# Performance work log

Hardware: AMD Instinct MI355X
Metric: run time of the kernel (lower is better)

## Reference

```python
import jax, jax.numpy as jnp
import numpy as np

SPARSITY = 0.01  # sparsity_threshold (softshrink lambda)


def _cas(n):
    # Hartley cas kernel: cos + sin
    t = jnp.arange(n, dtype=jnp.float32)
    a = 2.0 * jnp.pi * jnp.outer(t, t) / n
    return jnp.cos(a) + jnp.sin(a)


def _dht2d(x):
    # Faithful to source 4-D branch: transforms the LAST TWO axes (W and C)
    B, H, W, C = x.shape
    y = jnp.einsum('bhwc,cd->bhwd', x, _cas(C))          # contract channel axis
    return jnp.einsum('vw,bhwd->bhvd', _cas(W), y)       # contract width axis


def setup_inputs() -> dict:
    key = jax.random.key(0)
    k0, k1, k2, k3, k4 = jax.random.split(key, 5)
    B, H, W, C = 1, 180, 360, 512
    nb, bs, f = 8, 64, 1  # num_blocks, block_size, hidden_size_factor
    scale = 0.02
    x = jax.random.normal(k0, (B, H, W, C), jnp.float32)
    w1 = scale * jax.random.normal(k1, (2, nb, bs, bs * f), jnp.float32)
    b1 = scale * jax.random.normal(k2, (2, nb, bs * f), jnp.float32)
    w2 = scale * jax.random.normal(k3, (2, nb, bs * f, bs), jnp.float32)
    b2 = scale * jax.random.normal(k4, (2, nb, bs), jnp.float32)
    return {"x": x, "w1": w1, "b1": b1, "w2": w2, "b2": b2}


def reference(x, w1, b1, w2, b2):
    bias = x
    B, H, W, C = x.shape
    nb, bs = w1.shape[1], w1.shape[2]

    xh = _dht2d(x).reshape(B, H, W, nb, bs)                       # X_H_k
    xn = jnp.roll(jnp.flip(xh, axis=(1, 2)), shift=(1, 1), axis=(1, 2))  # X_H_{-k}

    # layer 1: 0.5*(Xk(w0+w1) + Xn(w0-w1)) + b  (algebraic regroup of the 4 einsums)
    w1a, w1b = w1[0] + w1[1], w1[0] - w1[1]
    o1k = jax.nn.relu(0.5 * (jnp.einsum('bhwki,kio->bhwko', xh, w1a)
                             + jnp.einsum('bhwki,kio->bhwko', xn, w1b)) + b1[0])
    o1n = jax.nn.relu(0.5 * (jnp.einsum('bhwki,kio->bhwko', xn, w1a)
                             + jnp.einsum('bhwki,kio->bhwko', xh, w1b)) + b1[1])

    # layer 2 (faithfully reproduces source bug: o2n consumes o2k, bias included)
    w2a, w2b = w2[0] + w2[1], w2[0] - w2[1]
    o2k = 0.5 * (jnp.einsum('bhwki,kio->bhwko', o1k, w2a)
                 + jnp.einsum('bhwki,kio->bhwko', o1n, w2b)) + b2[0]
    o2n = 0.5 * (jnp.einsum('bhwki,kio->bhwko', o1n, w2a)
                 + jnp.einsum('bhwki,kio->bhwko', o2k, w2b)) + b2[1]

    y = (o2k + o2n).reshape(B, H, W, C)
    y = jnp.sign(y) * jax.nn.relu(jnp.abs(y) - SPARSITY)          # softshrink
    y = _dht2d(y) / (W * C)                                       # idht2d normalization
    return y + bias
```

## Files before the change

### kernel.cpp

```cpp
#include <hip/hip_runtime.h>
#include <math.h>

#define HH 180
#define WDIM 360
#define CDIM 512
#define NP 64800
#define PL 184320

typedef unsigned short u16;
typedef __attribute__((ext_vector_type(8))) short short8;
typedef __attribute__((ext_vector_type(4))) float f4;

__device__ __forceinline__ u16 f2bf(float f){
    unsigned u = __float_as_uint(f);
    return (u16)((u + 0x7fffu + ((u >> 16) & 1u)) >> 16);
}
__device__ __forceinline__ void gl_lds16(const void* g, void* l){
    __builtin_amdgcn_global_load_lds((const __attribute__((address_space(1))) void*)g,
                                     (__attribute__((address_space(3))) void*)l, 16, 0, 0);
}

__global__ void prep(const float* __restrict__ w1, const float* __restrict__ w2,
                     u16* __restrict__ casC, u16* __restrict__ casW, u16* __restrict__ wts)
{
    int idx = blockIdx.x * 256 + threadIdx.x;
    if (idx < 512*512){
        int i = idx >> 9, j = idx & 511;
        int m = (i * j) & 511;
        float a = (float)m * (6.283185307179586f / 512.0f);
        float s, c; __sincosf(a, &s, &c);
        casC[idx] = f2bf(c + s);
    }
    if (idx < 360*384){
        int i = idx / 384, j = idx - (idx / 384) * 384;
        u16 v = 0;
        if (j < 360){
            int m = (i * j) % 360;
            float a = (float)m * (6.283185307179586f / 360.0f);
            float s, c; __sincosf(a, &s, &c);
            v = f2bf(c + s);
        }
        casW[idx] = v;
    }
    if (idx < 131072){
        int s = idx >> 15, r = idx & 32767;
        int kb = r >> 12, o = (r >> 6) & 63, ii = r & 63;
        const float* w = (s < 2) ? w1 : w2;
        float v0 = w[kb*4096 + ii*64 + o];
        float v1 = w[32768 + kb*4096 + ii*64 + o];
        float v = 0.5f * ((s & 1) ? (v0 - v1) : (v0 + v1));
        wts[idx] = f2bf(v);
    }
}

template<int ASTAGE, int STORE, int SWAP>
__global__ __launch_bounds__(256)
void gemm_k(const void* __restrict__ A, int ldA, long long sA, int clampA,
            const u16* __restrict__ B, int ldB, long long sB,
            void* __restrict__ C, long long sC, int Mreal,
            const float* __restrict__ X, float scale, int nK)
{
    __shared__ u16 As[4096];
    __shared__ u16 Bs[4096];

    const int tid = threadIdx.x, wv = tid >> 6, l = tid & 63;
    const int l16 = l & 15, quad = l >> 4;
    const int z = blockIdx.z;
    const int bx = SWAP ? blockIdx.y : blockIdx.x;
    const int by = SWAP ? blockIdx.x : blockIdx.y;
    const int row0 = bx * 128, col0 = by * 128;

    const int rh = wv & 1, c0 = wv >> 1;

    const u16* gB = B + sB * z + (long long)(col0 + rh*64 + l) * ldB;
    u16* lB0 = Bs + c0*1024 + rh*512;
    u16* lB1 = lB0 + 2048;

    const u16* gA = nullptr; u16* lA0 = nullptr; u16* lA1 = nullptr;
    const float* gAf = nullptr; int arow = 0;
    if constexpr (ASTAGE == 0){
        int r = row0 + rh*64 + l; r = r <= clampA ? r : clampA;
        gA  = (const u16*)A + sA * z + (long long)r * ldA;
        lA0 = As + c0*1024 + rh*512;
        lA1 = lA0 + 2048;
    } else {
        int r = row0 + (tid >> 1); r = r <= clampA ? r : clampA;
        gAf  = (const float*)A + (long long)r * ldA + (tid & 1) * 16;
        arow = tid >> 1;
    }

    f4 acc[4][4];
    #pragma unroll
    for (int mt = 0; mt < 4; ++mt)
        #pragma unroll
        for (int nt = 0; nt < 4; ++nt)
            acc[mt][nt] = (f4)0.0f;

    const int mrow = (wv >> 1) * 64, ncol = (wv & 1) * 64;

    for (int kt = 0; kt < nK; ++kt){
        const int k0 = kt * 32;
        gl_lds16(gB + k0 + c0*8,     lB0);
        gl_lds16(gB + k0 + (c0+2)*8, lB1);
        if constexpr (ASTAGE == 0){
            gl_lds16(gA + k0 + c0*8,     lA0);
            gl_lds16(gA + k0 + (c0+2)*8, lA1);
        } else {
            const float* p = gAf + k0;
            float4 f0 = *(const float4*)(p);
            float4 f1 = *(const float4*)(p + 4);
            float4 f2 = *(const float4*)(p + 8);
            float4 f3 = *(const float4*)(p + 12);
            uint4 w0, w1;
            w0.x = (unsigned)f2bf(f0.x) | ((unsigned)f2bf(f0.y) << 16);
            w0.y = (unsigned)f2bf(f0.z) | ((unsigned)f2bf(f0.w) << 16);
            w0.z = (unsigned)f2bf(f1.x) | ((unsigned)f2bf(f1.y) << 16);
            w0.w = (unsigned)f2bf(f1.z) | ((unsigned)f2bf(f1.w) << 16);
            w1.x = (unsigned)f2bf(f2.x) | ((unsigned)f2bf(f2.y) << 16);
            w1.y = (unsigned)f2bf(f2.z) | ((unsigned)f2bf(f2.w) << 16);
            w1.z = (unsigned)f2bf(f3.x) | ((unsigned)f2bf(f3.y) << 16);
            w1.w = (unsigned)f2bf(f3.z) | ((unsigned)f2bf(f3.w) << 16);
            const int cb = (tid & 1) * 2;
            *(uint4*)&As[cb*1024       + arow*8] = w0;
            *(uint4*)&As[(cb+1)*1024   + arow*8] = w1;
        }
        __syncthreads();
        short8 af[4];
        #pragma unroll
        for (int mt = 0; mt < 4; ++mt)
            af[mt] = *(const short8*)&As[quad*1024 + (mrow + mt*16 + l16)*8];
        #pragma unroll
        for (int nt = 0; nt < 4; ++nt){
            short8 bfv = *(const short8*)&Bs[quad*1024 + (ncol + nt*16 + l16)*8];
            #pragma unroll
            for (int mt = 0; mt < 4; ++mt)
                acc[mt][nt] = __builtin_amdgcn_mfma_f32_16x16x32_bf16(af[mt], bfv, acc[mt][nt], 0, 0, 0);
        }
        __syncthreads();
    }

    #pragma unroll
    for (int mt = 0; mt < 4; ++mt){
        #pragma unroll
        for (int i = 0; i < 4; ++i){
            int gr = row0 + mrow + mt*16 + quad*4 + i;
            if (gr >= Mreal) continue;
            int th = 0, tw = 0;
            if constexpr (STORE == 1){ th = gr / 360; tw = gr - th * 360; }
            #pragma unroll
            for (int nt = 0; nt < 4; ++nt){
                int gc = col0 + ncol + nt*16 + l16;
                if constexpr (STORE == 0){
                    ((u16*)C)[sC*z + (long long)gr*512 + gc] = f2bf(acc[mt][nt][i]);
                } else if constexpr (STORE == 1){
                    ((u16*)C)[((long long)th*512 + gc)*360 + tw] = f2bf(acc[mt][nt][i]);
                } else {
                    long long off = sC*z + (long long)gr*512 + gc;
                    ((float*)C)[off] = fmaf(acc[mt][nt][i], scale, X[off]);
                }
            }
        }
    }
}

__global__ __launch_bounds__(256)
void mlp_k(const u16* __restrict__ xh, const u16* __restrict__ wts,
           const float* __restrict__ b1, const float* __restrict__ b2,
           u16* __restrict__ yout)
{
    __shared__ u16 sW0[64*72], sW1[64*72];
    __shared__ u16 sXh[64*72], sXn[64*72], s1k[64*72], s1n[64*72];
    __shared__ float sb[256];

    const int tid = threadIdx.x;
    const int wv = tid >> 6, l = tid & 63, lane16 = l & 15, quad = l >> 4;
    const int kb = blockIdx.y;
    const int p0 = blockIdx.x * 64;
    const int w16 = wv * 16;

    if (tid < 64){
        sb[tid]       = b1[kb*64 + tid];
        sb[64 + tid]  = b1[512 + kb*64 + tid];
        sb[128 + tid] = b2[kb*64 + tid];
        sb[192 + tid] = b2[512 + kb*64 + tid];
    }
    {
        const int r = tid >> 2, sg = (tid & 3) * 16;
        const u16* s0 = wts + kb*4096 + r*64 + sg;
        const u16* s1 = wts + 32768 + kb*4096 + r*64 + sg;
        *(uint4*)&sW0[r*72 + sg]     = *(const uint4*)s0;
        *(uint4*)&sW0[r*72 + sg + 8] = *(const uint4*)(s0 + 8);
        *(uint4*)&sW1[r*72 + sg]     = *(const uint4*)s1;
        *(uint4*)&sW1[r*72 + sg + 8] = *(const uint4*)(s1 + 8);

        int p = p0 + r; int pc = p <= 64799 ? p : 64799;
        int h = pc / 360; int v = pc - h * 360;
        int hn = (h == 0) ? 0 : (180 - h);
        int vn = (v == 0) ? 0 : (360 - v);
        long long bh = (long long)pc * 512 + kb*64 + sg;
        long long bn = (long long)(hn*360 + vn) * 512 + kb*64 + sg;
        *(uint4*)&sXh[r*72 + sg]     = *(const uint4*)&xh[bh];
        *(uint4*)&sXh[r*72 + sg + 8] = *(const uint4*)&xh[bh + 8];
        *(uint4*)&sXn[r*72 + sg]     = *(const uint4*)&xh[bn];
        *(uint4*)&sXn[r*72 + sg + 8] = *(const uint4*)&xh[bn + 8];
    }
    __syncthreads();

    f4 aK[4], aN[4];
    #pragma unroll
    for (int nt = 0; nt < 4; ++nt){ aK[nt] = (f4)0.0f; aN[nt] = (f4)0.0f; }
    #pragma unroll
    for (int kq = 0; kq < 2; ++kq){
        short8 fxh = *(const short8*)&sXh[(w16 + lane16)*72 + kq*32 + quad*8];
        short8 fxn = *(const short8*)&sXn[(w16 + lane16)*72 + kq*32 + quad*8];
        #pragma unroll
        for (int nt = 0; nt < 4; ++nt){
            short8 wa = *(const short8*)&sW0[(nt*16 + lane16)*72 + kq*32 + quad*8];
            short8 wb = *(const short8*)&sW1[(nt*16 + lane16)*72 + kq*32 + quad*8];
            aK[nt] = __builtin_amdgcn_mfma_f32_16x16x32_bf16(fxh, wa, aK[nt], 0,0,0);
            aK[nt] = __builtin_amdgcn_mfma_f32_16x16x32_bf16(fxn, wb, aK[nt], 0,0,0);
            aN[nt] = __builtin_amdgcn_mfma_f32_16x16x32_bf16(fxn, wa, aN[nt], 0,0,0);
            aN[nt] = __builtin_amdgcn_mfma_f32_16x16x32_bf16(fxh, wb, aN[nt], 0,0,0);
        }
    }
    #pragma unroll
    for (int nt = 0; nt < 4; ++nt){
        int cc = nt*16 + lane16;
        #pragma unroll
        for (int i = 0; i < 4; ++i){
            int rr = w16 + quad*4 + i;
            float vk = fmaxf(aK[nt][i] + sb[cc], 0.f);
            float vn = fmaxf(aN[nt][i] + sb[64 + cc], 0.f);
            s1k[rr*72 + cc] = f2bf(vk);
            s1n[rr*72 + cc] = f2bf(vn);
        }
    }
    __syncthreads();

    {
        const int r = tid >> 2, sg = (tid & 3) * 16;
        const u16* s0 = wts + 65536 + kb*4096 + r*64 + sg;
        const u16* s1 = wts + 98304 + kb*4096 + r*64 + sg;
        *(uint4*)&sW0[r*72 + sg]     = *(const uint4*)s0;
        *(uint4*)&sW0[r*72 + sg + 8] = *(const uint4*)(s0 + 8);
        *(uint4*)&sW1[r*72 + sg]     = *(const uint4*)s1;
        *(uint4*)&sW1[r*72 + sg + 8] = *(const uint4*)(s1 + 8);
    }
    __syncthreads();

    f4 k2[4];
    #pragma unroll
    for (int nt = 0; nt < 4; ++nt) k2[nt] = (f4)0.0f;
    #pragma unroll
    for (int kq = 0; kq < 2; ++kq){
        short8 a1k = *(const short8*)&s1k[(w16 + lane16)*72 + kq*32 + quad*8];
        short8 a1n = *(const short8*)&s1n[(w16 + lane16)*72 + kq*32 + quad*8];
        #pragma unroll
        for (int nt = 0; nt < 4; ++nt){
            short8 wa = *(const short8*)&sW0[(nt*16 + lane16)*72 + kq*32 + quad*8];
            short8 wb = *(const short8*)&sW1[(nt*16 + lane16)*72 + kq*32 + quad*8];
            k2[nt] = __builtin_amdgcn_mfma_f32_16x16x32_bf16(a1k, wa, k2[nt], 0,0,0);
            k2[nt] = __builtin_amdgcn_mfma_f32_16x16x32_bf16(a1n, wb, k2[nt], 0,0,0);
        }
    }
    #pragma unroll
    for (int nt = 0; nt < 4; ++nt){
        int cc = nt*16 + lane16;
        #pragma unroll
        for (int i = 0; i < 4; ++i){
            int rr = w16 + quad*4 + i;
            float v2 = k2[nt][i] + sb[128 + cc];
            k2[nt][i] = v2;
            sXh[rr*72 + cc] = f2bf(v2);
        }
    }
    __syncthreads();

    f4 n2[4];
    #pragma unroll
    for (int nt = 0; nt < 4; ++nt) n2[nt] = (f4)0.0f;
    #pragma unroll
    for (int kq = 0; kq < 2; ++kq){
        short8 a1n = *(const short8*)&s1n[(w16 + lane16)*72 + kq*32 + quad*8];
        short8 a2k = *(const short8*)&sXh[(w16 + lane16)*72 + kq*32 + quad*8];
        #pragma unroll
        for (int nt = 0; nt < 4; ++nt){
            short8 wa = *(const short8*)&sW0[(nt*16 + lane16)*72 + kq*32 + quad*8];
            short8 wb = *(const short8*)&sW1[(nt*16 + lane16)*72 + kq*32 + quad*8];
            n2[nt] = __builtin_amdgcn_mfma_f32_16x16x32_bf16(a1n, wa, n2[nt], 0,0,0);
            n2[nt] = __builtin_amdgcn_mfma_f32_16x16x32_bf16(a2k, wb, n2[nt], 0,0,0);
        }
    }
    #pragma unroll
    for (int nt = 0; nt < 4; ++nt){
        int cc = nt*16 + lane16;
        #pragma unroll
        for (int i = 0; i < 4; ++i){
            int rr = w16 + quad*4 + i;
            int p = p0 + rr;
            float y = k2[nt][i] + n2[nt][i] + sb[192 + cc];
            float ay = fabsf(y) - 0.01f;
            float r0 = ay > 0.f ? (y > 0.f ? ay : -ay) : 0.f;
            if (p < 64800) yout[(long long)p * 512 + kb*64 + cc] = f2bf(r0);
        }
    }
}

extern "C" void kernel_launch(void* const* d_in, const int* in_sizes, int n_in,
                              void* d_out, int out_size, void* d_ws, size_t ws_size,
                              hipStream_t stream) {
    const float* x  = (const float*)d_in[0];
    const float* w1 = (const float*)d_in[1];
    const float* b1 = (const float*)d_in[2];
    const float* w2 = (const float*)d_in[3];
    const float* b2 = (const float*)d_in[4];
    float* out = (float*)d_out;

    u16* ws   = (u16*)d_ws;
    u16* casC = ws;
    u16* casW = casC + 262144;
    u16* wts  = casW + 138240;
    u16* bufT = wts  + 131072;
    u16* bufP = bufT + 33177664;

    prep<<<1024, 256, 0, stream>>>(w1, w2, casC, casW, wts);

    dim3 gBig(4, 507, 1);
    dim3 gW(3, 4, 180);
    dim3 gM(1013, 8, 1);

    gemm_k<1,1,1><<<gBig, 256, 0, stream>>>(x, 512, 0, 64799,
                                            casC, 512, 0,
                                            bufT, 0, 64800, nullptr, 0.f, 16);
    gemm_k<0,0,0><<<gW, 256, 0, stream>>>(casW, 384, 0, 359,
                                          bufT, 360, (long long)PL,
                                          bufP, (long long)PL, 360, nullptr, 0.f, 12);
    mlp_k<<<gM, 256, 0, stream>>>(bufP, wts, b1, b2, bufT);
    gemm_k<0,1,1><<<gBig, 256, 0, stream>>>(bufT, 512, 0, 64799,
                                            casC, 512, 0,
                                            bufP, 0, 64800, nullptr, 0.f, 16);
    gemm_k<0,2,0><<<gW, 256, 0, stream>>>(casW, 384, 0, 359,
                                          bufP, 360, (long long)PL,
                                          out, (long long)PL, 360,
                                          x, 1.0f/184320.0f, 12);
}
```

Baseline: 718.7 us.

## Double-buffer GEMM LDS tiles and swizzle block order per XCD

The GEMM kernel now uses two LDS buffers, so the next K-slice's loads (direct-to-LDS, or fp32 register loads for the converting stage) are issued before the MFMAs on the current slice, leaving one barrier per iteration. The big channel-transform GEMMs also switch to a 1-D grid whose block index is remapped so that consecutive tiles land on the same XCD, aiming for better L2 reuse of the A rows. This doubles LDS use per block, which may lower occupancy, and holds the prefetched fp32 registers across the MFMA loop.

```diff
diff --git a/kernel.cpp b/kernel.cpp
--- a/kernel.cpp
+++ b/kernel.cpp
@@ -58,35 +58,43 @@
 void gemm_k(const void* __restrict__ A, int ldA, long long sA, int clampA,
             const u16* __restrict__ B, int ldB, long long sB,
             void* __restrict__ C, long long sC, int Mreal,
-            const float* __restrict__ X, float scale, int nK)
+            const float* __restrict__ X, float scale, int nK, int nbx)
 {
-    __shared__ u16 As[4096];
-    __shared__ u16 Bs[4096];
+    __shared__ u16 As[2][4096];
+    __shared__ u16 Bs[2][4096];
 
     const int tid = threadIdx.x, wv = tid >> 6, l = tid & 63;
     const int l16 = l & 15, quad = l >> 4;
     const int z = blockIdx.z;
-    const int bx = SWAP ? blockIdx.y : blockIdx.x;
-    const int by = SWAP ? blockIdx.x : blockIdx.y;
+
+    int bx, by;
+    if constexpr (SWAP){
+        int n = gridDim.x;
+        int q = n >> 3, r = n & 7;
+        int xcd = blockIdx.x & 7, idx = blockIdx.x >> 3;
+        int swz = (xcd < r ? xcd*(q+1) : r*(q+1) + (xcd-r)*q) + idx;
+        bx = swz / nbx;
+        by = swz - bx * nbx;
+    } else {
+        bx = blockIdx.x;
+        by = blockIdx.y;
+    }
     const int row0 = bx * 128, col0 = by * 128;
 
     const int rh = wv & 1, c0 = wv >> 1;
 
     const u16* gB = B + sB * z + (long long)(col0 + rh*64 + l) * ldB;
-    u16* lB0 = Bs + c0*1024 + rh*512;
-    u16* lB1 = lB0 + 2048;
-
-    const u16* gA = nullptr; u16* lA0 = nullptr; u16* lA1 = nullptr;
-    const float* gAf = nullptr; int arow = 0;
+
+    const u16* gA = nullptr;
+    const float* gAf = nullptr; int arow = 0, cb = 0;
     if constexpr (ASTAGE == 0){
         int r = row0 + rh*64 + l; r = r <= clampA ? r : clampA;
-        gA  = (const u16*)A + sA * z + (long long)r * ldA;
-        lA0 = As + c0*1024 + rh*512;
-        lA1 = lA0 + 2048;
+        gA = (const u16*)A + sA * z + (long long)r * ldA;
     } else {
         int r = row0 + (tid >> 1); r = r <= clampA ? r : clampA;
         gAf  = (const float*)A + (long long)r * ldA + (tid & 1) * 16;
         arow = tid >> 1;
+        cb   = (tid & 1) * 2;
     }
 
     f4 acc[4][4];
@@ -98,45 +106,71 @@
 
     const int mrow = (wv >> 1) * 64, ncol = (wv & 1) * 64;
 
+    float4 f0, f1, f2, f3;
+
+    auto stageB = [&](int buf, int k0){
+        gl_lds16(gB + k0 + c0*8,     &Bs[buf][c0*1024     + rh*512]);
+        gl_lds16(gB + k0 + (c0+2)*8, &Bs[buf][(c0+2)*1024 + rh*512]);
+    };
+    auto stageA = [&](int buf, int k0){
+        gl_lds16(gA + k0 + c0*8,     &As[buf][c0*1024     + rh*512]);
+        gl_lds16(gA + k0 + (c0+2)*8, &As[buf][(c0+2)*1024 + rh*512]);
+    };
+    auto issueA = [&](int k0){
+        const float* p = gAf + k0;
+        f0 = *(const float4*)(p);
+        f1 = *(const float4*)(p + 4);
+        f2 = *(const float4*)(p + 8);
+        f3 = *(const float4*)(p + 12);
+    };
+    auto writeA = [&](int buf){
+        uint4 w0, w1;
+        w0.x = (unsigned)f2bf(f0.x) | ((unsigned)f2bf(f0.y) << 16);
+        w0.y = (unsigned)f2bf(f0.z) | ((unsigned)f2bf(f0.w) << 16);
+        w0.z = (unsigned)f2bf(f1.x) | ((unsigned)f2bf(f1.y) << 16);
+        w0.w = (unsigned)f2bf(f1.z) | ((unsigned)f2bf(f1.w) << 16);
+        w1.x = (unsigned)f2bf(f2.x) | ((unsigned)f2bf(f2.y) << 16);
+        w1.y = (unsigned)f2bf(f2.z) | ((unsigned)f2bf(f2.w) << 16);
+        w1.z = (unsigned)f2bf(f3.x) | ((unsigned)f2bf(f3.y) << 16);
+        w1.w = (unsigned)f2bf(f3.z) | ((unsigned)f2bf(f3.w) << 16);
+        *(uint4*)&As[buf][cb*1024     + arow*8] = w0;
+        *(uint4*)&As[buf][(cb+1)*1024 + arow*8] = w1;
+    };
+
+    stageB(0, 0);
+    if constexpr (ASTAGE == 0){
+        stageA(0, 0);
+    } else {
+        issueA(0);
+        writeA(0);
+    }
+    __syncthreads();
+
+    int cur = 0;
     for (int kt = 0; kt < nK; ++kt){
-        const int k0 = kt * 32;
-        gl_lds16(gB + k0 + c0*8,     lB0);
-        gl_lds16(gB + k0 + (c0+2)*8, lB1);
-        if constexpr (ASTAGE == 0){
-            gl_lds16(gA + k0 + c0*8,     lA0);
-            gl_lds16(gA + k0 + (c0+2)*8, lA1);
-        } else {
-            const float* p = gAf + k0;
-            float4 f0 = *(const float4*)(p);
-            float4 f1 = *(const float4*)(p + 4);
-            float4 f2 = *(const float4*)(p + 8);
-            float4 f3 = *(const float4*)(p + 12);
-            uint4 w0, w1;
-            w0.x = (unsigned)f2bf(f0.x) | ((unsigned)f2bf(f0.y) << 16);
-            w0.y = (unsigned)f2bf(f0.z) | ((unsigned)f2bf(f0.w) << 16);
-            w0.z = (unsigned)f2bf(f1.x) | ((unsigned)f2bf(f1.y) << 16);
-            w0.w = (unsigned)f2bf(f1.z) | ((unsigned)f2bf(f1.w) << 16);
-            w1.x = (unsigned)f2bf(f2.x) | ((unsigned)f2bf(f2.y) << 16);
-            w1.y = (unsigned)f2bf(f2.z) | ((unsigned)f2bf(f2.w) << 16);
-            w1.z = (unsigned)f2bf(f3.x) | ((unsigned)f2bf(f3.y) << 16);
-            w1.w = (unsigned)f2bf(f3.z) | ((unsigned)f2bf(f3.w) << 16);
-            const int cb = (tid & 1) * 2;
-            *(uint4*)&As[cb*1024       + arow*8] = w0;
-            *(uint4*)&As[(cb+1)*1024   + arow*8] = w1;
-        }
-        __syncthreads();
+        const bool more = (kt + 1 < nK);
+        const int k0n = (kt + 1) * 32;
+        if (more){
+            stageB(cur ^ 1, k0n);
+            if constexpr (ASTAGE == 0) stageA(cur ^ 1, k0n);
+            else                       issueA(k0n);
+        }
         short8 af[4];
         #pragma unroll
         for (int mt = 0; mt < 4; ++mt)
-            af[mt] = *(const short8*)&As[quad*1024 + (mrow + mt*16 + l16)*8];
+            af[mt] = *(const short8*)&As[cur][quad*1024 + (mrow + mt*16 + l16)*8];
         #pragma unroll
         for (int nt = 0; nt < 4; ++nt){
-            short8 bfv = *(const short8*)&Bs[quad*1024 + (ncol + nt*16 + l16)*8];
+            short8 bfv = *(const short8*)&Bs[cur][quad*1024 + (ncol + nt*16 + l16)*8];
             #pragma unroll
             for (int mt = 0; mt < 4; ++mt)
                 acc[mt][nt] = __builtin_amdgcn_mfma_f32_16x16x32_bf16(af[mt], bfv, acc[mt][nt], 0, 0, 0);
         }
+        if constexpr (ASTAGE == 1){
+            if (more) writeA(cur ^ 1);
+        }
         __syncthreads();
+        cur ^= 1;
     }
 
     #pragma unroll
@@ -325,22 +359,22 @@
 
     prep<<<1024, 256, 0, stream>>>(w1, w2, casC, casW, wts);
 
-    dim3 gBig(4, 507, 1);
+    dim3 gBig(2028, 1, 1);
     dim3 gW(3, 4, 180);
     dim3 gM(1013, 8, 1);
 
     gemm_k<1,1,1><<<gBig, 256, 0, stream>>>(x, 512, 0, 64799,
                                             casC, 512, 0,
-                                            bufT, 0, 64800, nullptr, 0.f, 16);
+                                            bufT, 0, 64800, nullptr, 0.f, 16, 4);
     gemm_k<0,0,0><<<gW, 256, 0, stream>>>(casW, 384, 0, 359,
                                           bufT, 360, (long long)PL,
-                                          bufP, (long long)PL, 360, nullptr, 0.f, 12);
+                                          bufP, (long long)PL, 360, nullptr, 0.f, 12, 1);
     mlp_k<<<gM, 256, 0, stream>>>(bufP, wts, b1, b2, bufT);
     gemm_k<0,1,1><<<gBig, 256, 0, stream>>>(bufT, 512, 0, 64799,
                                             casC, 512, 0,
-                                            bufP, 0, 64800, nullptr, 0.f, 16);
+                                            bufP, 0, 64800, nullptr, 0.f, 16, 4);
     gemm_k<0,2,0><<<gW, 256, 0, stream>>>(casW, 384, 0, 359,
                                           bufP, 360, (long long)PL,
                                           out, (long long)PL, 360,
-                                          x, 1.0f/184320.0f, 12);
-}
+                                          x, 1.0f/184320.0f, 12, 1);
+}
```

Measured after the change: 706.8 us. No clear change (-1.6%).
